# Kernel tuning notes

Measured on AMD Instinct MI355X. Metric: run time of the kernel, lower is better.

Reference implementation:

```python
import jax, jax.numpy as jnp
import numpy as np

NUM_QUBITS = 24
GATE_QUBITS = 4
NUM_STEPS = 8
GATE_DIM = 2 ** GATE_QUBITS  # 16


def setup_inputs() -> dict:
    key = jax.random.key(0)
    k1, k2 = jax.random.split(key)
    # statevector: leading dim 2 = (real, imag), then one size-2 axis per qubit
    state = jax.random.normal(k1, (2,) + (2,) * NUM_QUBITS, dtype=jnp.float32)
    # gates: [steps, 2(re/im), 2^k, 2^k]
    gates = jax.random.normal(k2, (NUM_STEPS, 2, GATE_DIM, GATE_DIM), dtype=jnp.float32)
    # distinct qubit indices per step (static permutation metadata)
    rng = np.random.default_rng(0)
    targets = np.stack(
        [rng.choice(NUM_QUBITS, size=GATE_QUBITS, replace=False) for _ in range(NUM_STEPS)]
    ).astype(np.int64)
    return {"state": state, "targets": targets, "gates": gates}


def _apply_gates(state, gates, targets):
    n = NUM_QUBITS
    dims = list(range(n))
    for step in range(targets.shape[0]):
        target = [int(q) for q in targets[step]]
        # qubit q lives on axis (n-1-q) of the qubit block; reversed as in source
        target_axes = list(reversed([n - 1 - q for q in target]))
        perm = [i for i in dims if i not in target_axes] + target_axes
        perm = [0] + [i + 1 for i in perm]  # keep re/im axis in front
        inv_perm = [0] * (n + 1)
        for i, d in enumerate(perm):
            inv_perm[d] = i
        # gather target qubits into the last axis, flatten the rest
        s = jnp.transpose(state, perm).reshape(2, -1, GATE_DIM)
        sr, si = s[0], s[1]
        gr, gi = gates[step, 0], gates[step, 1]
        # complex matmul: state @ gate^T, (a+bi)(c+di) split into re/im
        nr = sr @ gr.T - si @ gi.T
        ni = sr @ gi.T + si @ gr.T
        state = jnp.transpose(
            jnp.stack([nr, ni]).reshape((2,) + (2,) * n), inv_perm
        )
    return state


def reference(state, targets, gates):
    return _apply_gates(state, gates, np.asarray(targets))
```

## Files before the change

kernel.cpp:

```cpp
#include <hip/hip_runtime.h>

#define N_QUBITS 24
#define NSTATE (1u << N_QUBITS)
#define GDIM 16

__global__ __launch_bounds__(256) void apply_gate4(
    const float* src, float* dst,
    const int* __restrict__ targets_raw,
    const float* __restrict__ gates,
    int step)
{
    __shared__ float gsh[2 * GDIM * GDIM];
    __shared__ int tsh[4];
    __shared__ int ssh[4];

    const int tid = threadIdx.x;

    const float* G = gates + (size_t)step * 512;
    {
        int i = tid;
        if (i < 256) {
            gsh[2 * i]     = G[i];
            gsh[2 * i + 1] = G[256 + i];
        }
    }

    if (tid == 0) {
        bool is64 = true;
        for (int i = 0; i < 32; ++i) {
            if (targets_raw[2 * i + 1] != 0) { is64 = false; break; }
        }
        int t[4];
        #pragma unroll
        for (int j = 0; j < 4; ++j) {
            t[j] = is64 ? targets_raw[2 * (step * 4 + j)]
                        : targets_raw[step * 4 + j];
            tsh[j] = t[j];
        }
        #pragma unroll
        for (int a = 0; a < 3; ++a)
            #pragma unroll
            for (int b = a + 1; b < 4; ++b)
                if (t[b] < t[a]) { int tmp = t[a]; t[a] = t[b]; t[b] = tmp; }
        #pragma unroll
        for (int j = 0; j < 4; ++j) ssh[j] = t[j];
    }
    __syncthreads();

    const int t0 = tsh[0], t1 = tsh[1], t2 = tsh[2], t3 = tsh[3];

    unsigned base = blockIdx.x * 256u + (unsigned)tid;
    #pragma unroll
    for (int j = 0; j < 4; ++j) {
        const unsigned s = (unsigned)ssh[j];
        const unsigned low = base & ((1u << s) - 1u);
        base = ((base >> s) << (s + 1)) | low;
    }

    float sr[GDIM], si[GDIM];
    unsigned idx[GDIM];
    #pragma unroll
    for (int g = 0; g < GDIM; ++g) {
        const unsigned o = ((unsigned)(g & 1)        << t0)
                         | ((unsigned)((g >> 1) & 1) << t1)
                         | ((unsigned)((g >> 2) & 1) << t2)
                         | ((unsigned)((g >> 3) & 1) << t3);
        const unsigned id = base | o;
        idx[g] = id;
        sr[g] = src[id];
        si[g] = src[NSTATE + id];
    }

    #pragma unroll
    for (int g = 0; g < GDIM; ++g) {
        float ar = 0.f, ai = 0.f;
        #pragma unroll
        for (int h = 0; h < GDIM; ++h) {
            const float gr = gsh[2 * (g * GDIM + h)];
            const float gi = gsh[2 * (g * GDIM + h) + 1];
            ar = fmaf(gr, sr[h], ar);
            ar = fmaf(-gi, si[h], ar);
            ai = fmaf(gr, si[h], ai);
            ai = fmaf(gi, sr[h], ai);
        }
        dst[idx[g]] = ar;
        dst[NSTATE + idx[g]] = ai;
    }
}

extern "C" void kernel_launch(void* const* d_in, const int* in_sizes, int n_in,
                              void* d_out, int out_size, void* d_ws, size_t ws_size,
                              hipStream_t stream) {
    const float* state   = (const float*)d_in[0];
    const int*   targets = (const int*)d_in[1];
    const float* gates   = (const float*)d_in[2];
    float* out = (float*)d_out;

    const int groups = NSTATE / GDIM;
    const dim3 block(256);
    const dim3 grid(groups / 256);

    apply_gate4<<<grid, block, 0, stream>>>(state, out, targets, gates, 0);
    for (int s = 1; s < 8; ++s) {
        apply_gate4<<<grid, block, 0, stream>>>(out, out, targets, gates, s);
    }
}
```

Before: 604.5 us.

## Stage 4096-amplitude tiles in LDS with coalesced float4 global access

Each block now loads a contiguous tile spanning the target qubits plus the lowest non-target qubits into shared memory with vectorized float4 loads. It applies the 16x16 complex gate from LDS using an XOR swizzle to reduce bank conflicts, then writes the tile back coalesced. This replaces scattered per-thread strided global gathers and scatters. It adds LDS traffic and two extra barriers, and marks src/dst restrict even though later launches alias them.

```diff
diff --git a/kernel.cpp b/kernel.cpp
--- a/kernel.cpp
+++ b/kernel.cpp
@@ -3,27 +3,27 @@
 #define N_QUBITS 24
 #define NSTATE (1u << N_QUBITS)
 #define GDIM 16
+#define TILE_BITS 12
+#define TILE (1u << TILE_BITS)
 
 __global__ __launch_bounds__(256) void apply_gate4(
-    const float* src, float* dst,
+    const float* __restrict__ src, float* __restrict__ dst,
     const int* __restrict__ targets_raw,
     const float* __restrict__ gates,
     int step)
 {
     __shared__ float gsh[2 * GDIM * GDIM];
-    __shared__ int tsh[4];
-    __shared__ int ssh[4];
+    __shared__ float ldsR[TILE];
+    __shared__ float ldsI[TILE];
+    __shared__ int s12sh[12];
+    __shared__ int possh[4];
+    __shared__ int ntpossh[8];
 
     const int tid = threadIdx.x;
 
     const float* G = gates + (size_t)step * 512;
-    {
-        int i = tid;
-        if (i < 256) {
-            gsh[2 * i]     = G[i];
-            gsh[2 * i + 1] = G[256 + i];
-        }
-    }
+    gsh[2 * tid]     = G[tid];
+    gsh[2 * tid + 1] = G[256 + tid];
 
     if (tid == 0) {
         bool is64 = true;
@@ -31,46 +31,80 @@
             if (targets_raw[2 * i + 1] != 0) { is64 = false; break; }
         }
         int t[4];
+        unsigned tmask = 0;
         #pragma unroll
         for (int j = 0; j < 4; ++j) {
             t[j] = is64 ? targets_raw[2 * (step * 4 + j)]
                         : targets_raw[step * 4 + j];
-            tsh[j] = t[j];
+            tmask |= 1u << t[j];
+        }
+        unsigned smask = tmask;
+        int cnt = 0;
+        for (int b = 0; b < N_QUBITS && cnt < 8; ++b)
+            if (!((tmask >> b) & 1u)) { smask |= 1u << b; ++cnt; }
+        int k = 0, k2 = 0;
+        for (int b = 0; b < N_QUBITS; ++b) {
+            if ((smask >> b) & 1u) {
+                s12sh[k] = b;
+                if (!((tmask >> b) & 1u)) ntpossh[k2++] = k;
+                ++k;
+            }
         }
         #pragma unroll
-        for (int a = 0; a < 3; ++a)
-            #pragma unroll
-            for (int b = a + 1; b < 4; ++b)
-                if (t[b] < t[a]) { int tmp = t[a]; t[a] = t[b]; t[b] = tmp; }
-        #pragma unroll
-        for (int j = 0; j < 4; ++j) ssh[j] = t[j];
+        for (int j = 0; j < 4; ++j)
+            possh[j] = __popc(smask & ((1u << t[j]) - 1u));
     }
     __syncthreads();
 
-    const int t0 = tsh[0], t1 = tsh[1], t2 = tsh[2], t3 = tsh[3];
+    unsigned base = blockIdx.x;
+    #pragma unroll
+    for (int i = 0; i < 12; ++i) {
+        const unsigned s = (unsigned)s12sh[i];
+        base = ((base >> s) << (s + 1)) | (base & ((1u << s) - 1u));
+    }
+    const unsigned sh8 = s12sh[8], sh9 = s12sh[9],
+                   sh10 = s12sh[10], sh11 = s12sh[11];
 
-    unsigned base = blockIdx.x * 256u + (unsigned)tid;
+    unsigned addr4[4], w4[4];
     #pragma unroll
-    for (int j = 0; j < 4; ++j) {
-        const unsigned s = (unsigned)ssh[j];
-        const unsigned low = base & ((1u << s) - 1u);
-        base = ((base >> s) << (s + 1)) | low;
+    for (int p = 0; p < 4; ++p) {
+        const unsigned a = (unsigned)(tid * 4 + p * 1024);
+        addr4[p] = base
+                 | (a & 255u)
+                 | (((a >> 8) & 1u) << sh8)
+                 | (((a >> 9) & 1u) << sh9)
+                 | (((a >> 10) & 1u) << sh10)
+                 | (((a >> 11) & 1u) << sh11);
+        w4[p] = a ^ (((a >> 5) & 7u) << 2);
     }
 
+    #pragma unroll
+    for (int p = 0; p < 4; ++p) {
+        *(float4*)(ldsR + w4[p]) = *(const float4*)(src + addr4[p]);
+        *(float4*)(ldsI + w4[p]) = *(const float4*)(src + NSTATE + addr4[p]);
+    }
+    __syncthreads();
+
+    unsigned gb = 0;
+    #pragma unroll
+    for (int i = 0; i < 8; ++i)
+        gb |= (((unsigned)tid >> i) & 1u) << ntpossh[i];
+    const int p0 = possh[0], p1 = possh[1], p2 = possh[2], p3 = possh[3];
+
+    unsigned aa[GDIM];
     float sr[GDIM], si[GDIM];
-    unsigned idx[GDIM];
     #pragma unroll
-    for (int g = 0; g < GDIM; ++g) {
-        const unsigned o = ((unsigned)(g & 1)        << t0)
-                         | ((unsigned)((g >> 1) & 1) << t1)
-                         | ((unsigned)((g >> 2) & 1) << t2)
-                         | ((unsigned)((g >> 3) & 1) << t3);
-        const unsigned id = base | o;
-        idx[g] = id;
-        sr[g] = src[id];
-        si[g] = src[NSTATE + id];
+    for (int h = 0; h < GDIM; ++h) {
+        const unsigned a = gb
+            | (((unsigned)h & 1u) << p0)
+            | ((((unsigned)h >> 1) & 1u) << p1)
+            | ((((unsigned)h >> 2) & 1u) << p2)
+            | ((((unsigned)h >> 3) & 1u) << p3);
+        const unsigned w = a ^ (((a >> 5) & 7u) << 2);
+        aa[h] = w;
+        sr[h] = ldsR[w];
+        si[h] = ldsI[w];
     }
-
     #pragma unroll
     for (int g = 0; g < GDIM; ++g) {
         float ar = 0.f, ai = 0.f;
@@ -83,8 +117,15 @@
             ai = fmaf(gr, si[h], ai);
             ai = fmaf(gi, sr[h], ai);
         }
-        dst[idx[g]] = ar;
-        dst[NSTATE + idx[g]] = ai;
+        ldsR[aa[g]] = ar;
+        ldsI[aa[g]] = ai;
+    }
+    __syncthreads();
+
+    #pragma unroll
+    for (int p = 0; p < 4; ++p) {
+        *(float4*)(dst + addr4[p])          = *(const float4*)(ldsR + w4[p]);
+        *(float4*)(dst + NSTATE + addr4[p]) = *(const float4*)(ldsI + w4[p]);
     }
 }
 
@@ -96,9 +137,8 @@
     const float* gates   = (const float*)d_in[2];
     float* out = (float*)d_out;
 
-    const int groups = NSTATE / GDIM;
     const dim3 block(256);
-    const dim3 grid(groups / 256);
+    const dim3 grid(NSTATE / TILE);
 
     apply_gate4<<<grid, block, 0, stream>>>(state, out, targets, gates, 0);
     for (int s = 1; s < 8; ++s) {
```

Measured after the change: 580.5 us. 1.04x faster.

## Fuse consecutive gates into LDS-tiled sweeps planned on device

Applied to the files above, without the earlier changes.

Adds a device-side planning kernel that groups consecutive 4-qubit gates whose combined target qubits fit into a 13-qubit tile. Each sweep kernel loads an 8192-amplitude tile into swizzled LDS once and applies all gates in the group there. It then writes the tile back with vectorized float4 accesses. The aim is to cut global memory passes over the 128 MiB statevector from eight to at most four. In exchange it adds a planning launch, LDS pressure and barriers, and gate coefficients are read from global memory inside the inner loop.

```diff
diff --git a/kernel.cpp b/kernel.cpp
--- a/kernel.cpp
+++ b/kernel.cpp
@@ -1,90 +1,157 @@
 #include <hip/hip_runtime.h>
 
-#define N_QUBITS 24
-#define NSTATE (1u << N_QUBITS)
-#define GDIM 16
+#define NQ 24
+#define NSTATE (1u << NQ)
+#define TB 13
+#define TILE (1u << TB)
+#define NTHR 512
+#define SWEEP_STRIDE 288
+#define META_HDR 16
 
-__global__ __launch_bounds__(256) void apply_gate4(
-    const float* src, float* dst,
-    const int* __restrict__ targets_raw,
-    const float* __restrict__ gates,
-    int step)
+
+__global__ void plan_kernel(const int* __restrict__ targets_raw, int* __restrict__ meta)
 {
-    __shared__ float gsh[2 * GDIM * GDIM];
-    __shared__ int tsh[4];
-    __shared__ int ssh[4];
+    if (threadIdx.x != 0 || blockIdx.x != 0) return;
+    bool is64 = true;
+    for (int i = 0; i < 4; ++i)
+        if (targets_raw[2 * i + 1] != 0) { is64 = false; break; }
 
-    const int tid = threadIdx.x;
-
-    const float* G = gates + (size_t)step * 512;
-    {
-        int i = tid;
-        if (i < 256) {
-            gsh[2 * i]     = G[i];
-            gsh[2 * i + 1] = G[256 + i];
+    int t[8][4]; unsigned tm[8];
+    for (int s = 0; s < 8; ++s) {
+        unsigned m = 0;
+        for (int j = 0; j < 4; ++j) {
+            int v = is64 ? targets_raw[2 * (s * 4 + j)] : targets_raw[s * 4 + j];
+            t[s][j] = v; m |= 1u << v;
         }
+        tm[s] = m;
     }
 
-    if (tid == 0) {
-        bool is64 = true;
-        for (int i = 0; i < 32; ++i) {
-            if (targets_raw[2 * i + 1] != 0) { is64 = false; break; }
+    int ng = 0, sp = 0;
+    while (sp < 8) {
+        unsigned mask = 0xFu;
+        int cnt = 0, steps[8];
+        while (sp < 8 && cnt < 8) {
+            unsigned nm = mask | tm[sp];
+            if (__popc(nm) <= TB) { mask = nm; steps[cnt++] = sp++; }
+            else break;
         }
-        int t[4];
-        #pragma unroll
-        for (int j = 0; j < 4; ++j) {
-            t[j] = is64 ? targets_raw[2 * (step * 4 + j)]
-                        : targets_raw[step * 4 + j];
-            tsh[j] = t[j];
+        unsigned sm = mask;
+        int need = TB - __popc(sm);
+        for (int b = 0; b < NQ && need > 0; ++b)
+            if (!((sm >> b) & 1u)) { sm |= 1u << b; --need; }
+
+        int* base = meta + META_HDR + ng * SWEEP_STRIDE;
+        base[0] = cnt;
+        int spos[NQ]; int si = 0;
+        for (int b = 0; b < NQ; ++b) {
+            if ((sm >> b) & 1u) { spos[b] = si; base[1 + si] = b; ++si; }
+            else spos[b] = -1;
         }
-        #pragma unroll
-        for (int a = 0; a < 3; ++a)
-            #pragma unroll
-            for (int b = a + 1; b < 4; ++b)
-                if (t[b] < t[a]) { int tmp = t[a]; t[a] = t[b]; t[b] = tmp; }
-        #pragma unroll
-        for (int j = 0; j < 4; ++j) ssh[j] = t[j];
+        for (int k = 0; k < cnt; ++k) {
+            int st = steps[k];
+            int* gk = base + 16 + k * 32;
+            gk[0] = st;
+            int pt[4];
+            for (int j = 0; j < 4; ++j) pt[j] = spos[t[st][j]];
+            for (int h = 0; h < 16; ++h)
+                gk[1 + h] = ((h & 1) << pt[0]) | (((h >> 1) & 1) << pt[1])
+                          | (((h >> 2) & 1) << pt[2]) | (((h >> 3) & 1) << pt[3]);
+            const unsigned tmask =
+                (1u << pt[0]) | (1u << pt[1]) | (1u << pt[2]) | (1u << pt[3]);
+            int idx = 0;
+            for (int pos = 0; pos < TB; ++pos)
+                if (!((tmask >> pos) & 1u)) gk[17 + idx++] = pos;
+        }
+        ++ng;
+    }
+    meta[0] = ng;
+}
+
+__global__ __launch_bounds__(NTHR) void sweep_k(
+    const float* __restrict__ src, float* __restrict__ dst,
+    const float* __restrict__ gates, const int* __restrict__ meta, int sweep)
+{
+    if (sweep >= meta[0]) return;
+
+    __shared__ float lds[TILE * 2];
+    const int tid = threadIdx.x;
+    const int* sb = meta + META_HDR + sweep * SWEEP_STRIDE;
+    const int ngat = sb[0];
+
+    unsigned base = blockIdx.x;
+    #pragma unroll
+    for (int i = 0; i < TB; ++i) {
+        const unsigned s = (unsigned)sb[1 + i];
+        base = ((base >> s) << (s + 1)) | (base & ((1u << s) - 1u));
+    }
+    unsigned ga0 = base | ((unsigned)(tid * 4) & 15u);
+    #pragma unroll
+    for (int i = 0; i < 7; ++i)
+        ga0 |= (((unsigned)tid >> (2 + i)) & 1u) << sb[5 + i];
+
+    unsigned ga_[4], w_[4];
+    #pragma unroll
+    for (int c = 0; c < 4; ++c) {
+        ga_[c] = ga0 | (((unsigned)c & 1u) << sb[12])
+                     | ((((unsigned)c >> 1) & 1u) << sb[13]);
+        const unsigned a = (unsigned)(c * 2048 + tid * 4);
+        w_[c] = a ^ (((a >> 7) & 0x1Fu) << 2);
+    }
+
+    #pragma unroll
+    for (int c = 0; c < 4; ++c) {
+        const float4 r4 = *(const float4*)(src + ga_[c]);
+        const float4 i4 = *(const float4*)(src + NSTATE + ga_[c]);
+        float* p = lds + 2 * w_[c];
+        ((float4*)p)[0] = make_float4(r4.x, i4.x, r4.y, i4.y);
+        ((float4*)p)[1] = make_float4(r4.z, i4.z, r4.w, i4.w);
     }
     __syncthreads();
 
-    const int t0 = tsh[0], t1 = tsh[1], t2 = tsh[2], t3 = tsh[3];
+    for (int k = 0; k < ngat; ++k) {
+        const int* gk = sb + 16 + k * 32;
+        const int step = __builtin_amdgcn_readfirstlane(gk[0]);
+        const float* __restrict__ Gre = gates + (size_t)step * 512;
+        const float* __restrict__ Gim = Gre + 256;
 
-    unsigned base = blockIdx.x * 256u + (unsigned)tid;
-    #pragma unroll
-    for (int j = 0; j < 4; ++j) {
-        const unsigned s = (unsigned)ssh[j];
-        const unsigned low = base & ((1u << s) - 1u);
-        base = ((base >> s) << (s + 1)) | low;
-    }
+        unsigned gb = 0;
+        #pragma unroll
+        for (int i = 0; i < 9; ++i)
+            gb |= (((unsigned)tid >> i) & 1u) << gk[17 + i];
 
-    float sr[GDIM], si[GDIM];
-    unsigned idx[GDIM];
-    #pragma unroll
-    for (int g = 0; g < GDIM; ++g) {
-        const unsigned o = ((unsigned)(g & 1)        << t0)
-                         | ((unsigned)((g >> 1) & 1) << t1)
-                         | ((unsigned)((g >> 2) & 1) << t2)
-                         | ((unsigned)((g >> 3) & 1) << t3);
-        const unsigned id = base | o;
-        idx[g] = id;
-        sr[g] = src[id];
-        si[g] = src[NSTATE + id];
+        float sr[16], si[16]; unsigned aw[16];
+        #pragma unroll
+        for (int h = 0; h < 16; ++h) {
+            const unsigned idx = gb | (unsigned)gk[1 + h];
+            const unsigned w = idx ^ (((idx >> 7) & 0x1Fu) << 2);
+            aw[h] = w;
+            const float2 v = *(const float2*)(lds + 2 * w);
+            sr[h] = v.x; si[h] = v.y;
+        }
+        #pragma unroll
+        for (int g = 0; g < 16; ++g) {
+            float ar = 0.f, ai = 0.f;
+            #pragma unroll
+            for (int h = 0; h < 16; ++h) {
+                const float grv = Gre[g * 16 + h];
+                const float giv = Gim[g * 16 + h];
+                ar = fmaf(grv, sr[h], ar);
+                ar = fmaf(-giv, si[h], ar);
+                ai = fmaf(grv, si[h], ai);
+                ai = fmaf(giv, sr[h], ai);
+            }
+            *(float2*)(lds + 2 * aw[g]) = make_float2(ar, ai);
+        }
+        __syncthreads();
     }
 
     #pragma unroll
-    for (int g = 0; g < GDIM; ++g) {
-        float ar = 0.f, ai = 0.f;
-        #pragma unroll
-        for (int h = 0; h < GDIM; ++h) {
-            const float gr = gsh[2 * (g * GDIM + h)];
-            const float gi = gsh[2 * (g * GDIM + h) + 1];
-            ar = fmaf(gr, sr[h], ar);
-            ar = fmaf(-gi, si[h], ar);
-            ai = fmaf(gr, si[h], ai);
-            ai = fmaf(gi, sr[h], ai);
-        }
-        dst[idx[g]] = ar;
-        dst[NSTATE + idx[g]] = ai;
+    for (int c = 0; c < 4; ++c) {
+        const float* p = lds + 2 * w_[c];
+        const float4 q0 = ((const float4*)p)[0];
+        const float4 q1 = ((const float4*)p)[1];
+        *(float4*)(dst + ga_[c])          = make_float4(q0.x, q0.z, q1.x, q1.z);
+        *(float4*)(dst + NSTATE + ga_[c]) = make_float4(q0.y, q0.w, q1.y, q1.w);
     }
 }
 
@@ -95,13 +162,14 @@
     const int*   targets = (const int*)d_in[1];
     const float* gates   = (const float*)d_in[2];
     float* out = (float*)d_out;
+    int* meta = (int*)d_ws;
 
-    const int groups = NSTATE / GDIM;
-    const dim3 block(256);
-    const dim3 grid(groups / 256);
+    plan_kernel<<<1, 64, 0, stream>>>(targets, meta);
 
-    apply_gate4<<<grid, block, 0, stream>>>(state, out, targets, gates, 0);
-    for (int s = 1; s < 8; ++s) {
-        apply_gate4<<<grid, block, 0, stream>>>(out, out, targets, gates, s);
-    }
+    const dim3 block(NTHR);
+    const dim3 grid(NSTATE / TILE);
+
+    sweep_k<<<grid, block, 0, stream>>>(state, out, gates, meta, 0);
+    for (int s = 1; s < 4; ++s)
+        sweep_k<<<grid, block, 0, stream>>>(out, out, gates, meta, s);
 }
```

After: 495.8 us. 1.22x faster.
